# Kernel tuning notes

Measured on AMD Instinct MI355X. Metric: run time of the kernel, lower is better.

The kernel has to match this reference:

```python
import jax, jax.numpy as jnp
import numpy as np

B, P, M, CI, CO, W = 8, 16384, 16, 16, 32, 17
RES_RATE = 0.5
SQ_CONV = float(np.sqrt(1.0 - RES_RATE))
SQ_RES = float(np.sqrt(RES_RATE))


def setup_inputs() -> dict:
    key = jax.random.key(0)
    k0, k1, k2, k3, k4 = jax.random.split(key, 5)
    in_pc = jax.random.normal(k0, (B, P, CI), dtype=jnp.float32)
    # neighbor ids in [0, P]; value P is the padding sentinel (masked out)
    neighbor_id = jax.random.randint(k1, (P, M), 0, P + 1)
    weights = jax.random.normal(k2, (W, CO * CI), dtype=jnp.float32)
    bias = jnp.zeros((P, CO), dtype=jnp.float32)  # perpoint_bias == 1
    w_weights = jax.random.normal(k3, (P, M, W), dtype=jnp.float32) / (M * W)
    weight_res = jax.random.normal(k4, (CO, CI), dtype=jnp.float32) / CO
    return {
        "in_pc": in_pc,
        "weights": weights,
        "bias": bias,
        "w_weights": w_weights,
        "weight_res": weight_res,
        "neighbor_id": neighbor_id,
    }


def reference(in_pc, weights, bias, w_weights, weight_res, neighbor_id):
    b = in_pc.shape[0]
    # mask: 1 for real neighbor, 0 for padding sentinel (id == P)
    mask = (neighbor_id != P).astype(in_pc.dtype)  # [P, M]
    # pad point cloud with one zero point so sentinel index gathers zeros
    in_pc_pad = jnp.concatenate(
        [in_pc, jnp.zeros((b, 1, CI), dtype=in_pc.dtype)], axis=1
    )  # [B, P+1, CI]
    in_neighbors = in_pc_pad[:, neighbor_id]  # [B, P, M, CI]
    # per-point conv weights: masked learned combination of basis weights
    ww = w_weights * mask[:, :, None]  # [P, M, W]
    Wpm = jnp.einsum("pmw,wc->pmc", ww, weights).reshape(P, M, CO, CI)
    # gather-generate-matmul: contract neighbors with per-point weights, sum over M
    out_pc_conv = jnp.einsum("pmoi,bpmi->bpo", Wpm, in_neighbors) + bias
    out_pc_conv = jax.nn.elu(out_pc_conv)  # not final layer
    # residual branch: channel projection (in_c != out_c), identity over points
    out_pc_res = jnp.einsum("oi,bpi->bpo", weight_res, in_pc_pad)[:, :P]
    return out_pc_conv * SQ_CONV + out_pc_res * SQ_RES
```

## Files before the change

kernel.cpp:

```cpp
#include <hip/hip_runtime.h>

#define PP 16384
#define SQH 0.70710678118654752440f

typedef unsigned int u32;
typedef unsigned short u16;
typedef __attribute__((ext_vector_type(8))) short bfrag;
typedef __attribute__((ext_vector_type(4))) float ffrag;
typedef __attribute__((ext_vector_type(16))) float ffrag16;
typedef __attribute__((ext_vector_type(4))) float f4;

union BU { bfrag v; uint4 u; };

__device__ __forceinline__ u32 pk2(float a, float b) {
  u32 ua = __float_as_uint(a), ub = __float_as_uint(b);
  return ((ua + 0x8000u) >> 16) | ((ub + 0x8000u) & 0xffff0000u);
}

#define XTB_B ((size_t)(PP + 1) * 256)
#define WB_B  XTB_B
#define WR_B  (XTB_B + 18432)
#define XG_B  (WR_B + 2048)
#define XG_W  (XG_B / 4)

__global__ __launch_bounds__(256) void prep_kernel(
    const float* __restrict__ in_pc, const float* __restrict__ weights,
    const float* __restrict__ weight_res, u32* __restrict__ ws) {
  __shared__ u32 T[64 * 72];
  const int blk = blockIdx.x, t = threadIdx.x;
  if (blk < 256) {
    const int p0 = blk * 64;
    const int pl = t >> 2, i4 = t & 3;
#pragma unroll
    for (int b = 0; b < 8; ++b) {
      f4 v = *(const f4*)(in_pc + ((size_t)b * PP + p0 + pl) * 16 + i4 * 4);
      T[pl * 72 + b * 8 + i4 * 2]     = pk2(v.x, v.y);
      T[pl * 72 + b * 8 + i4 * 2 + 1] = pk2(v.z, v.w);
    }
    __syncthreads();
#pragma unroll
    for (int k = 0; k < 4; ++k) {
      int idx = k * 256 + t;
      int pl2 = idx >> 4, c2 = (idx & 15) * 4;
      uint4 v = *(const uint4*)&T[pl2 * 72 + c2];
      *(uint4*)&ws[(size_t)(p0 + pl2) * 64 + c2] = v;
    }
#pragma unroll
    for (int k = 0; k < 4; ++k) {
      int idx = k * 256 + t;
      int pl2 = idx >> 4, m = idx & 15;
      u32 T0 = T[pl2 * 72 + m];
      u32 T1 = T[pl2 * 72 + 16 + m];
      u32 T2 = T[pl2 * 72 + 32 + m];
      u32 T3 = T[pl2 * 72 + 48 + m];
      uint4 w;
      w.x = (T0 & 0xffffu) | (T1 << 16);
      w.y = (T2 & 0xffffu) | (T3 << 16);
      w.z = (T0 >> 16)     | (T1 & 0xffff0000u);
      w.w = (T2 >> 16)     | (T3 & 0xffff0000u);
      *(uint4*)&ws[XG_W + (size_t)(p0 + pl2) * 64 + m * 4] = w;
    }
    return;
  }
  if (blk == 256 && t < 32) {
    *(uint2*)&ws[(size_t)PP * 64 + t * 2] = make_uint2(0u, 0u);
    *(uint2*)&ws[XG_W + (size_t)PP * 64 + t * 2] = make_uint2(0u, 0u);
  }
  int e = (blk - 256) * 256 + t;
  if (e < 1152) {
    int nt = e / 576, rem = e - nt * 576;
    int ks = rem >> 6, l = rem & 63;
    int quad = l >> 4, n = l & 15;
    int k0 = ks * 32 + quad * 8;
    uint4 pkd = make_uint4(0u, 0u, 0u, 0u);
    if (k0 < 272) {
      int w = k0 >> 4, i0 = k0 & 15;
      const float* src = weights + w * 512 + (nt * 16 + n) * 16 + i0;
      f4 lo = *(const f4*)src;
      f4 hi = *(const f4*)(src + 4);
      pkd = make_uint4(pk2(lo.x, lo.y), pk2(lo.z, lo.w), pk2(hi.x, hi.y), pk2(hi.z, hi.w));
    }
    *(uint4*)((char*)ws + WB_B + (size_t)e * 16) = pkd;
  } else if (e < 1280) {
    int l2 = e - 1152, nt = l2 >> 6, l = l2 & 63;
    int quad = l >> 4, n = l & 15;
    uint4 pkd = make_uint4(0u, 0u, 0u, 0u);
    if (quad < 2) {
      const float* src = weight_res + (nt * 16 + n) * 16 + quad * 8;
      f4 lo = *(const f4*)src;
      f4 hi = *(const f4*)(src + 4);
      pkd = make_uint4(pk2(lo.x, lo.y), pk2(lo.z, lo.w), pk2(hi.x, hi.y), pk2(hi.z, hi.w));
    }
    *(uint4*)((char*)ws + WR_B + (size_t)(e - 1152) * 16) = pkd;
  }
}

__device__ __forceinline__ void gather_pt(u32 (&ad)[4][4], const int (&nd)[16],
                                          const u16* __restrict__ xG,
                                          int h, int col) {
#pragma unroll
  for (int j = 0; j < 4; ++j) {
    uint2 d = *(const uint2*)(xG + (size_t)nd[h * 8 + 2 * j] * 128 + col * 4);
    uint2 e = *(const uint2*)(xG + (size_t)nd[h * 8 + 2 * j + 1] * 128 + col * 4);
    ad[0][j] = (d.x & 0xffffu) | (e.x << 16);
    ad[1][j] = (d.x >> 16)     | (e.x & 0xffff0000u);
    ad[2][j] = (d.y & 0xffffu) | (e.y << 16);
    ad[3][j] = (d.y >> 16)     | (e.y & 0xffff0000u);
  }
}

__global__ __launch_bounds__(256, 4) void pconv_main(
    const u32* __restrict__ ws,
    const float* __restrict__ bias,
    const float* __restrict__ wwg,
    const int*  __restrict__ nidg,
    float* __restrict__ out)
{
  __shared__ __attribute__((aligned(16))) u16 Abuf[4 * 16 * 296];

  const u16*  __restrict__ xTb = (const u16*)ws;
  const u16*  __restrict__ xG  = (const u16*)((const char*)ws + XG_B);
  const uint4* __restrict__ WB = (const uint4*)((const char*)ws + WB_B);
  const uint4* __restrict__ WR = (const uint4*)((const char*)ws + WR_B);

  const int tid = threadIdx.x;
  const int wid = __builtin_amdgcn_readfirstlane(tid >> 6);
  const int lane = tid & 63;
  const int lo16 = lane & 15, quad = lane >> 4;
  const int col = lane & 31, h = lane >> 5;
  u16* __restrict__ Aw = Abuf + wid * (16 * 296);

  const int p0 = (blockIdx.x * 4 + wid) * 2;

  {
    int r = lane >> 2, c = lane & 3;
    *(uint2*)(Aw + r * 296 + 272 + c * 4) = make_uint2(0u, 0u);
  }

  int nid0[16], nid1[16];
#pragma unroll
  for (int m = 0; m < 16; ++m) nid0[m] = nidg[(size_t)p0 * 16 + m];
#pragma unroll
  for (int m = 0; m < 16; ++m) nid1[m] = nidg[(size_t)(p0 + 1) * 16 + m];

  BU bb0, bb1;
  {
    float v0[8], v1[8];
#pragma unroll
    for (int idx = 0; idx < 8; ++idx) {
      float x0 = 0.f, x1 = 0.f;
      if (col < 17) {
        x0 = wwg[(size_t)p0 * 272 + (h * 8 + idx) * 17 + col];
        x1 = wwg[(size_t)(p0 + 1) * 272 + (h * 8 + idx) * 17 + col];
      }
      v0[idx] = x0; v1[idx] = x1;
    }
    bb0.u = make_uint4(pk2(v0[0], v0[1]), pk2(v0[2], v0[3]), pk2(v0[4], v0[5]), pk2(v0[6], v0[7]));
    bb1.u = make_uint4(pk2(v1[0], v1[1]), pk2(v1[2], v1[3]), pk2(v1[4], v1[5]), pk2(v1[6], v1[7]));
  }

  u32 a0[4][4], a1[4][4];
  gather_pt(a0, nid0, xG, h, col);
  gather_pt(a1, nid1, xG, h, col);

  float blo[4], bhi[4];
#pragma unroll
  for (int j = 0; j < 4; ++j) {
    int p_e = p0 + ((quad * 4 + j) >> 3);
    blo[j] = bias[(size_t)p_e * 32 + lo16];
    bhi[j] = bias[(size_t)p_e * 32 + 16 + lo16];
  }
  BU su;
  su.u = make_uint4(0u, 0u, 0u, 0u);
  {
    const int p_r = p0 + (lo16 >> 3), b_r = lo16 & 7;
    if (quad < 2)
      su.u = *(const uint4*)(xTb + (size_t)p_r * 128 + b_r * 16 + quad * 8);
  }
  BU rb0, rb1;
  rb0.u = WR[lane];
  rb1.u = WR[64 + lane];

#pragma unroll
  for (int pt = 0; pt < 2; ++pt) {
    const u32 (&ad)[4][4] = pt ? a1 : a0;
    BU bb = pt ? bb1 : bb0;
#pragma unroll
    for (int t = 0; t < 4; ++t) {
      BU aa;
      aa.u = make_uint4(ad[t][0], ad[t][1], ad[t][2], ad[t][3]);
      ffrag16 c = {};
      c = __builtin_amdgcn_mfma_f32_32x32x16_bf16(aa.v, bb.v, c, 0, 0, 0);
      if (col < 17) {
#pragma unroll
        for (int q = 0; q < 4; ++q) {
          int r = pt * 8 + 2 * t + (q >> 1);
          int i0 = 4 * h + 8 * (q & 1);
          u16* dst = Aw + r * 296 + col * 16 + i0;
          *(uint2*)dst = make_uint2(pk2(c[4 * q + 0], c[4 * q + 1]),
                                    pk2(c[4 * q + 2], c[4 * q + 3]));
        }
      }
    }
  }

  ffrag acc0 = {0.f, 0.f, 0.f, 0.f}, acc1 = {0.f, 0.f, 0.f, 0.f};
#pragma unroll
  for (int ks = 0; ks < 9; ++ks) {
    bfrag af = *(const bfrag*)(Aw + lo16 * 296 + ks * 32 + quad * 8);
    BU b0, b1;
    b0.u = WB[ks * 64 + lane];
    b1.u = WB[576 + ks * 64 + lane];
    acc0 = __builtin_amdgcn_mfma_f32_16x16x32_bf16(af, b0.v, acc0, 0, 0, 0);
    acc1 = __builtin_amdgcn_mfma_f32_16x16x32_bf16(af, b1.v, acc1, 0, 0, 0);
  }
  ffrag rz = {0.f, 0.f, 0.f, 0.f};
  ffrag res0 = __builtin_amdgcn_mfma_f32_16x16x32_bf16(su.v, rb0.v, rz, 0, 0, 0);
  ffrag res1 = __builtin_amdgcn_mfma_f32_16x16x32_bf16(su.v, rb1.v, rz, 0, 0, 0);

  float* Ef = (float*)Aw;
#pragma unroll
  for (int j = 0; j < 4; ++j) {
    int r = quad * 4 + j;
    float c0 = acc0[j] + blo[j];
    float c1 = acc1[j] + bhi[j];
    float e0 = c0 > 0.f ? c0 : (__expf(c0) - 1.f);
    float e1 = c1 > 0.f ? c1 : (__expf(c1) - 1.f);
    Ef[r * 40 + lo16]      = SQH * e0 + SQH * res0[j];
    Ef[r * 40 + 16 + lo16] = SQH * e1 + SQH * res1[j];
  }
#pragma unroll
  for (int k = 0; k < 2; ++k) {
    int rr = (lane >> 3) + 8 * k;
    int cc = lane & 7;
    f4 v = *(const f4*)(Ef + rr * 40 + cc * 4);
    int p_s = p0 + (rr >> 3), b_s = rr & 7;
    *(f4*)(out + ((size_t)b_s * PP + p_s) * 32 + cc * 4) = v;
  }
}

extern "C" void kernel_launch(void* const* d_in, const int* in_sizes, int n_in,
                              void* d_out, int out_size, void* d_ws, size_t ws_size,
                              hipStream_t stream) {
  const float* in_pc       = (const float*)d_in[0];
  const float* weights     = (const float*)d_in[1];
  const float* bias        = (const float*)d_in[2];
  const float* w_weights   = (const float*)d_in[3];
  const float* weight_res  = (const float*)d_in[4];
  const int*   neighbor_id = (const int*)d_in[5];
  float* out = (float*)d_out;
  u32* ws = (u32*)d_ws;

  hipLaunchKernelGGL(prep_kernel, dim3(261), dim3(256), 0, stream,
                     in_pc, weights, weight_res, ws);
  hipLaunchKernelGGL(pconv_main, dim3(2048), dim3(256), 0, stream,
                     ws, bias, w_weights, neighbor_id, out);
}
```

Baseline: 104.5 us.

## Process one point per wave to cut registers and raise occupancy

Each wave now handles a single point instead of two. This halves the neighbor-id, gathered-feature and LDS staging footprint, and allows a launch bound of 6 waves-per-EU with twice the blocks. The aim is more waves in flight to hide the latency of the random neighbor gathers. In exchange, the second-stage 16-row MFMAs now use only 8 valid rows, so weight loads and matrix instructions per point roughly double.

After: 124.6 us. 19.2% more time.

```diff
diff --git a/kernel.cpp b/kernel.cpp
--- a/kernel.cpp
+++ b/kernel.cpp
@@ -109,14 +109,14 @@
   }
 }
 
-__global__ __launch_bounds__(256, 4) void pconv_main(
+__global__ __launch_bounds__(256, 6) void pconv_main(
     const u32* __restrict__ ws,
     const float* __restrict__ bias,
     const float* __restrict__ wwg,
     const int*  __restrict__ nidg,
     float* __restrict__ out)
 {
-  __shared__ __attribute__((aligned(16))) u16 Abuf[4 * 16 * 296];
+  __shared__ __attribute__((aligned(16))) u16 Abuf[4 * 8 * 296];
 
   const u16*  __restrict__ xTb = (const u16*)ws;
   const u16*  __restrict__ xG  = (const u16*)((const char*)ws + XG_B);
@@ -128,86 +128,69 @@
   const int lane = tid & 63;
   const int lo16 = lane & 15, quad = lane >> 4;
   const int col = lane & 31, h = lane >> 5;
-  u16* __restrict__ Aw = Abuf + wid * (16 * 296);
-
-  const int p0 = (blockIdx.x * 4 + wid) * 2;
-
-  {
+  u16* __restrict__ Aw = Abuf + wid * (8 * 296);
+
+  const int p = blockIdx.x * 4 + wid;
+
+  if (lane < 32) {
     int r = lane >> 2, c = lane & 3;
     *(uint2*)(Aw + r * 296 + 272 + c * 4) = make_uint2(0u, 0u);
   }
 
-  int nid0[16], nid1[16];
-#pragma unroll
-  for (int m = 0; m < 16; ++m) nid0[m] = nidg[(size_t)p0 * 16 + m];
-#pragma unroll
-  for (int m = 0; m < 16; ++m) nid1[m] = nidg[(size_t)(p0 + 1) * 16 + m];
-
-  BU bb0, bb1;
+  int nid[16];
+#pragma unroll
+  for (int m = 0; m < 16; ++m) nid[m] = nidg[(size_t)p * 16 + m];
+
+  BU bb;
   {
-    float v0[8], v1[8];
+    float v[8];
 #pragma unroll
     for (int idx = 0; idx < 8; ++idx) {
-      float x0 = 0.f, x1 = 0.f;
-      if (col < 17) {
-        x0 = wwg[(size_t)p0 * 272 + (h * 8 + idx) * 17 + col];
-        x1 = wwg[(size_t)(p0 + 1) * 272 + (h * 8 + idx) * 17 + col];
-      }
-      v0[idx] = x0; v1[idx] = x1;
-    }
-    bb0.u = make_uint4(pk2(v0[0], v0[1]), pk2(v0[2], v0[3]), pk2(v0[4], v0[5]), pk2(v0[6], v0[7]));
-    bb1.u = make_uint4(pk2(v1[0], v1[1]), pk2(v1[2], v1[3]), pk2(v1[4], v1[5]), pk2(v1[6], v1[7]));
-  }
-
-  u32 a0[4][4], a1[4][4];
-  gather_pt(a0, nid0, xG, h, col);
-  gather_pt(a1, nid1, xG, h, col);
-
-  float blo[4], bhi[4];
-#pragma unroll
-  for (int j = 0; j < 4; ++j) {
-    int p_e = p0 + ((quad * 4 + j) >> 3);
-    blo[j] = bias[(size_t)p_e * 32 + lo16];
-    bhi[j] = bias[(size_t)p_e * 32 + 16 + lo16];
-  }
+      float x = 0.f;
+      if (col < 17)
+        x = wwg[(size_t)p * 272 + (h * 8 + idx) * 17 + col];
+      v[idx] = x;
+    }
+    bb.u = make_uint4(pk2(v[0], v[1]), pk2(v[2], v[3]),
+                      pk2(v[4], v[5]), pk2(v[6], v[7]));
+  }
+
+  u32 a[4][4];
+  gather_pt(a, nid, xG, h, col);
+
+  float blo = bias[(size_t)p * 32 + lo16];
+  float bhi = bias[(size_t)p * 32 + 16 + lo16];
   BU su;
   su.u = make_uint4(0u, 0u, 0u, 0u);
-  {
-    const int p_r = p0 + (lo16 >> 3), b_r = lo16 & 7;
-    if (quad < 2)
-      su.u = *(const uint4*)(xTb + (size_t)p_r * 128 + b_r * 16 + quad * 8);
-  }
+  if (quad < 2)
+    su.u = *(const uint4*)(xTb + (size_t)p * 128 + (lo16 & 7) * 16 + quad * 8);
   BU rb0, rb1;
   rb0.u = WR[lane];
   rb1.u = WR[64 + lane];
 
 #pragma unroll
-  for (int pt = 0; pt < 2; ++pt) {
-    const u32 (&ad)[4][4] = pt ? a1 : a0;
-    BU bb = pt ? bb1 : bb0;
-#pragma unroll
-    for (int t = 0; t < 4; ++t) {
-      BU aa;
-      aa.u = make_uint4(ad[t][0], ad[t][1], ad[t][2], ad[t][3]);
-      ffrag16 c = {};
-      c = __builtin_amdgcn_mfma_f32_32x32x16_bf16(aa.v, bb.v, c, 0, 0, 0);
-      if (col < 17) {
-#pragma unroll
-        for (int q = 0; q < 4; ++q) {
-          int r = pt * 8 + 2 * t + (q >> 1);
-          int i0 = 4 * h + 8 * (q & 1);
-          u16* dst = Aw + r * 296 + col * 16 + i0;
-          *(uint2*)dst = make_uint2(pk2(c[4 * q + 0], c[4 * q + 1]),
-                                    pk2(c[4 * q + 2], c[4 * q + 3]));
-        }
+  for (int t = 0; t < 4; ++t) {
+    BU aa;
+    aa.u = make_uint4(a[t][0], a[t][1], a[t][2], a[t][3]);
+    ffrag16 c = {};
+    c = __builtin_amdgcn_mfma_f32_32x32x16_bf16(aa.v, bb.v, c, 0, 0, 0);
+    if (col < 17) {
+#pragma unroll
+      for (int q = 0; q < 4; ++q) {
+        int r = 2 * t + (q >> 1);
+        int i0 = 4 * h + 8 * (q & 1);
+        u16* dst = Aw + r * 296 + col * 16 + i0;
+        *(uint2*)dst = make_uint2(pk2(c[4 * q + 0], c[4 * q + 1]),
+                                  pk2(c[4 * q + 2], c[4 * q + 3]));
       }
     }
   }
 
+  const int arow = lo16 & 7;
   ffrag acc0 = {0.f, 0.f, 0.f, 0.f}, acc1 = {0.f, 0.f, 0.f, 0.f};
 #pragma unroll
   for (int ks = 0; ks < 9; ++ks) {
-    bfrag af = *(const bfrag*)(Aw + lo16 * 296 + ks * 32 + quad * 8);
+    bfrag af = *(const bfrag*)(Aw + arow * 296 + ks * 32 + quad * 8);
     BU b0, b1;
     b0.u = WB[ks * 64 + lane];
     b1.u = WB[576 + ks * 64 + lane];
@@ -219,23 +202,22 @@
   ffrag res1 = __builtin_amdgcn_mfma_f32_16x16x32_bf16(su.v, rb1.v, rz, 0, 0, 0);
 
   float* Ef = (float*)Aw;
-#pragma unroll
-  for (int j = 0; j < 4; ++j) {
-    int r = quad * 4 + j;
-    float c0 = acc0[j] + blo[j];
-    float c1 = acc1[j] + bhi[j];
-    float e0 = c0 > 0.f ? c0 : (__expf(c0) - 1.f);
-    float e1 = c1 > 0.f ? c1 : (__expf(c1) - 1.f);
-    Ef[r * 40 + lo16]      = SQH * e0 + SQH * res0[j];
-    Ef[r * 40 + 16 + lo16] = SQH * e1 + SQH * res1[j];
-  }
-#pragma unroll
-  for (int k = 0; k < 2; ++k) {
-    int rr = (lane >> 3) + 8 * k;
-    int cc = lane & 7;
+  if (quad < 2) {
+#pragma unroll
+    for (int j = 0; j < 4; ++j) {
+      int r = quad * 4 + j;
+      float c0 = acc0[j] + blo;
+      float c1 = acc1[j] + bhi;
+      float e0 = c0 > 0.f ? c0 : (__expf(c0) - 1.f);
+      float e1 = c1 > 0.f ? c1 : (__expf(c1) - 1.f);
+      Ef[r * 40 + lo16]      = SQH * e0 + SQH * res0[j];
+      Ef[r * 40 + 16 + lo16] = SQH * e1 + SQH * res1[j];
+    }
+  }
+  {
+    int rr = lane >> 3, cc = lane & 7;
     f4 v = *(const f4*)(Ef + rr * 40 + cc * 4);
-    int p_s = p0 + (rr >> 3), b_s = rr & 7;
-    *(f4*)(out + ((size_t)b_s * PP + p_s) * 32 + cc * 4) = v;
+    *(f4*)(out + ((size_t)rr * PP + p) * 32 + cc * 4) = v;
   }
 }
 
@@ -253,6 +235,6 @@
 
   hipLaunchKernelGGL(prep_kernel, dim3(261), dim3(256), 0, stream,
                      in_pc, weights, weight_res, ws);
-  hipLaunchKernelGGL(pconv_main, dim3(2048), dim3(256), 0, stream,
+  hipLaunchKernelGGL(pconv_main, dim3(4096), dim3(256), 0, stream,
                      ws, bias, w_weights, neighbor_id, out);
 }
```
